# Kernel tuning notes

Hardware: AMD Instinct MI355X
Metric: run time of the kernel (lower is better)

## Reference

```python
import jax, jax.numpy as jnp
import numpy as np

N = 20000        # total atoms (atomic environments)
NFEAT = 2784     # power-spectrum feature size: sum_l n_max[l]^2 * n_pseudo^2
P = 4            # n_pseudo (alchemical pseudo-species)
H = 256          # MLP hidden width
S = 500          # number of structures
NSPEC = 8        # number of chemical species (len(all_species))
AVG_ATOMS = N / S  # average_number_of_atoms used for energy normalization


def setup_inputs() -> dict:
    key = jax.random.key(0)
    ks = jax.random.split(key, 8)
    features = jax.random.normal(ks[0], (N, NFEAT), dtype=jnp.float32)
    species = jax.random.randint(ks[1], (N,), 0, NSPEC)
    structure_idx = jax.random.randint(ks[2], (N,), 0, S)
    # combination matrix: Linear(n_species -> n_pseudo), no bias
    W_comb = jax.random.normal(ks[3], (NSPEC, P), dtype=jnp.float32) / np.float32(np.sqrt(NSPEC))
    # per-pseudo-species MLP weights (bias=False throughout)
    W1 = jax.random.normal(ks[4], (P, NFEAT, H), dtype=jnp.float32) / np.float32(np.sqrt(NFEAT))
    W2 = jax.random.normal(ks[5], (P, H, H), dtype=jnp.float32) / np.float32(np.sqrt(H))
    W3 = jax.random.normal(ks[6], (P, H, H), dtype=jnp.float32) / np.float32(np.sqrt(H))
    W4 = jax.random.normal(ks[7], (P, H, 1), dtype=jnp.float32) / np.float32(np.sqrt(H))
    return {"features": features, "W_comb": W_comb, "W1": W1, "W2": W2,
            "W3": W3, "W4": W4, "species": species, "structure_idx": structure_idx}


def reference(features, W_comb, W1, W2, W3, W4, species, structure_idx):
    # one-hot species encoding followed by combination_matrix linear map.
    # one_hot(species) @ W_comb  ==  W_comb[species]  (gather form, no [N, NSPEC] matmul)
    pseudo_w = W_comb[species]                                   # [N, P]
    # outer-product feature embedding: features[:, :, None] * pseudo_w[:, None, :]
    emb = features[:, :, None] * pseudo_w[:, None, :]            # [N, NFEAT, P]
    # per-pseudo-species MLP (Linear no-bias -> SiLU) x3 -> Linear to scalar,
    # vectorized over the pseudo dimension instead of a Python loop.
    h = jax.nn.silu(jnp.einsum('nfp,pfh->nph', emb, W1))         # [N, P, H]
    h = jax.nn.silu(jnp.einsum('nph,phk->npk', h, W2))           # [N, P, H]
    h = jax.nn.silu(jnp.einsum('nph,phk->npk', h, W3))           # [N, P, H]
    per_pseudo_e = jnp.einsum('nph,pho->npo', h, W4)[..., 0]     # [N, P]
    atomic_energies = per_pseudo_e.sum(axis=1) / np.float32(np.sqrt(P))  # [N]
    # scatter-add atomic energies into per-structure energies (index_add_)
    energies = jax.ops.segment_sum(atomic_energies, structure_idx, num_segments=S)
    return energies / np.float32(AVG_ATOMS)                     # [S]
```

## Files before the change

### kernel.cpp

```cpp
#include <hip/hip_runtime.h>
#include <hip/hip_bf16.h>
#include <stdint.h>

#define N_ATOMS 20000
#define NFEAT   2784
#define KP1     2880
#define KT1     45
#define SS      500
#define NPAD    20224
#define MCOLS   1024

typedef __attribute__((ext_vector_type(8))) short s16x8;
typedef __attribute__((ext_vector_type(4))) float f32x4;

static __device__ __forceinline__ unsigned short f2b(float f) {
    __hip_bfloat16 h = __float2bfloat16(f);
    return __builtin_bit_cast(unsigned short, h);
}
static __device__ __forceinline__ float b2f(unsigned short u) {
    unsigned int x = ((unsigned int)u) << 16;
    return __builtin_bit_cast(float, x);
}

#define GLOAD16(g, l) __builtin_amdgcn_global_load_lds( \
    (const __attribute__((address_space(1))) void*)(g), \
    (__attribute__((address_space(3))) void*)(l), 16, 0, 0)

__global__ void conv_feat(const float* __restrict__ F, unsigned short* __restrict__ out) {
    int row = blockIdx.x;
    int t = threadIdx.x;
    const float4* src = (const float4*)(F + (size_t)row * NFEAT);
    unsigned short* dst = out + (size_t)row * KP1;
    for (int g = t; g < KP1 / 4; g += 256) {
        float4 v;
        if (g < NFEAT / 4) v = src[g];
        else { v.x = 0.f; v.y = 0.f; v.z = 0.f; v.w = 0.f; }
        ushort4 o;
        o.x = f2b(v.x); o.y = f2b(v.y); o.z = f2b(v.z); o.w = f2b(v.w);
        *(ushort4*)(dst + g * 4) = o;
    }
}

__global__ void pack_w(const float* __restrict__ W, unsigned short* __restrict__ Bt,
                       int KD, int KP) {
    __shared__ unsigned short tile[32][256];
    int p = blockIdx.y;
    int f0 = blockIdx.x * 32;
    int t = threadIdx.x;
    #pragma unroll 4
    for (int i = 0; i < 32; ++i) {
        int f = f0 + i;
        float v = (f < KD) ? W[((size_t)p * KD + f) * 256 + t] : 0.f;
        tile[i][t] = f2b(v);
    }
    __syncthreads();
    unsigned short* drow = Bt + (size_t)(p * 256 + t) * KP + f0;
    #pragma unroll
    for (int i = 0; i < 32; i += 4) {
        ushort4 o;
        o.x = tile[i][t]; o.y = tile[i + 1][t]; o.z = tile[i + 2][t]; o.w = tile[i + 3][t];
        *(ushort4*)(drow + i) = o;
    }
}

__global__ void make_pw(const float* __restrict__ Wc, const int* __restrict__ spec,
                        float* __restrict__ pw) {
    int n = blockIdx.x * 256 + threadIdx.x;
    if (n < N_ATOMS) {
        int s = spec[n];
        float4 v = *(const float4*)(Wc + s * 4);
        *(float4*)(pw + n * 4) = v;
    }
}

__global__ void zero_f(float* o, int n) {
    int i = blockIdx.x * 256 + threadIdx.x;
    if (i < n) o[i] = 0.f;
}

__global__ __launch_bounds__(512, 4) void gemm1_pipe(
    const unsigned short* __restrict__ A,
    const unsigned short* __restrict__ Bt,
    const float* __restrict__ pw,
    unsigned short* __restrict__ C)
{
    __shared__ __align__(16) unsigned short lds_a[2 * 8192];
    __shared__ __align__(16) unsigned short lds_b[2 * 8192];

    int bid = blockIdx.x;
    int swz = (bid & 7) * 158 + (bid >> 3);
    int rowTile = swz >> 3;
    int colTile = swz & 7;
    int rowBase = rowTile * 128;
    int colBase = colTile * 128;
    int p = colTile >> 1;

    int t0 = threadIdx.x;
    int wave = t0 >> 6;
    int lane = t0 & 63;
    int wm = wave >> 1;
    int wn = wave & 1;

    int rA = t0 >> 3;
    int ckl = ((t0 & 7) ^ (rA & 7)) << 3;
    const unsigned short* sa = A + (size_t)(rowBase + rA) * KP1 + ckl;
    const unsigned short* sb = Bt + (size_t)(colBase + rA) * KP1 + ckl;

    int ra0 = wm * 32 + (lane & 15);
    int rb0 = wn * 64 + (lane & 15);
    int xr = lane & 7;
    int c0 = lane >> 4;

    f32x4 acc[2][4];
    f32x4 z4 = {0.f, 0.f, 0.f, 0.f};
    #pragma unroll
    for (int i = 0; i < 2; ++i)
        #pragma unroll
        for (int j = 0; j < 4; ++j) acc[i][j] = z4;

#define STAGE1(SB) do { \
    GLOAD16(sa,                     lds_a + (SB) * 8192 + t0 * 8); \
    GLOAD16(sa + (size_t)64 * KP1,  lds_a + (SB) * 8192 + 4096 + t0 * 8); \
    GLOAD16(sb,                     lds_b + (SB) * 8192 + t0 * 8); \
    GLOAD16(sb + (size_t)64 * KP1,  lds_b + (SB) * 8192 + 4096 + t0 * 8); \
    sa += 64; sb += 64; \
} while (0)

    STAGE1(0);
    STAGE1(1);
    asm volatile("s_waitcnt vmcnt(4)" ::: "memory");
    __builtin_amdgcn_s_barrier();
    __builtin_amdgcn_sched_barrier(0);

#define FSTEP(CB) do { \
    s16x8 af[2][2], bv[2][4]; \
    _Pragma("unroll") \
    for (int kk = 0; kk < 2; ++kk) { \
        int ch = ((((kk << 2) | c0) ^ xr) << 3); \
        _Pragma("unroll") \
        for (int fm = 0; fm < 2; ++fm) \
            af[kk][fm] = *(const s16x8*)&lds_a[(CB) * 8192 + (ra0 + fm * 16) * 64 + ch]; \
        _Pragma("unroll") \
        for (int fn = 0; fn < 4; ++fn) \
            bv[kk][fn] = *(const s16x8*)&lds_b[(CB) * 8192 + (rb0 + fn * 16) * 64 + ch]; \
    } \
    asm volatile("s_waitcnt lgkmcnt(0)" ::: "memory"); \
    __builtin_amdgcn_sched_barrier(0); \
    __builtin_amdgcn_s_barrier();             \
    __builtin_amdgcn_sched_barrier(0); \
    STAGE1(CB);                               \
    __builtin_amdgcn_s_setprio(1); \
    _Pragma("unroll") \
    for (int kk = 0; kk < 2; ++kk) \
        _Pragma("unroll") \
        for (int fm = 0; fm < 2; ++fm) \
            _Pragma("unroll") \
            for (int fn = 0; fn < 4; ++fn) \
                acc[fm][fn] = __builtin_amdgcn_mfma_f32_16x16x32_bf16( \
                    af[kk][fm], bv[kk][fn], acc[fm][fn], 0, 0, 0); \
    __builtin_amdgcn_s_setprio(0); \
    asm volatile("s_waitcnt vmcnt(4)" ::: "memory");    \
    __builtin_amdgcn_s_barrier(); \
    __builtin_amdgcn_sched_barrier(0); \
} while (0)

#define TSTEP(CB, DRAIN) do { \
    s16x8 af[2][2], bv[2][4]; \
    _Pragma("unroll") \
    for (int kk = 0; kk < 2; ++kk) { \
        int ch = ((((kk << 2) | c0) ^ xr) << 3); \
        _Pragma("unroll") \
        for (int fm = 0; fm < 2; ++fm) \
            af[kk][fm] = *(const s16x8*)&lds_a[(CB) * 8192 + (ra0 + fm * 16) * 64 + ch]; \
        _Pragma("unroll") \
        for (int fn = 0; fn < 4; ++fn) \
            bv[kk][fn] = *(const s16x8*)&lds_b[(CB) * 8192 + (rb0 + fn * 16) * 64 + ch]; \
    } \
    _Pragma("unroll") \
    for (int kk = 0; kk < 2; ++kk) \
        _Pragma("unroll") \
        for (int fm = 0; fm < 2; ++fm) \
            _Pragma("unroll") \
            for (int fn = 0; fn < 4; ++fn) \
                acc[fm][fn] = __builtin_amdgcn_mfma_f32_16x16x32_bf16( \
                    af[kk][fm], bv[kk][fn], acc[fm][fn], 0, 0, 0); \
    if (DRAIN) { \
        asm volatile("s_waitcnt vmcnt(0)" ::: "memory"); \
        __builtin_amdgcn_s_barrier(); \
        __builtin_amdgcn_sched_barrier(0); \
    } \
} while (0)

    for (int it = 0; it < 21; ++it) {
        FSTEP(0);
        FSTEP(1);
    }
    FSTEP(0);
    TSTEP(1, 1);
    TSTEP(0, 0);
#undef FSTEP
#undef TSTEP
#undef STAGE1

    int rGrp = (lane >> 4) << 2;
    int cLane = lane & 15;
    #pragma unroll
    for (int fm = 0; fm < 2; ++fm) {
        int r0 = rowBase + wm * 32 + fm * 16 + rGrp;
        float pwv[4];
        #pragma unroll
        for (int j = 0; j < 4; ++j) pwv[j] = pw[(size_t)(r0 + j) * 4 + p];
        #pragma unroll
        for (int fn = 0; fn < 4; ++fn) {
            int c = colBase + wn * 64 + fn * 16 + cLane;
            f32x4 a = acc[fm][fn];
            #pragma unroll
            for (int j = 0; j < 4; ++j) {
                float x = a[j] * pwv[j];
                float s = x / (1.f + __expf(-x));
                C[(size_t)(r0 + j) * MCOLS + c] = f2b(s);
            }
        }
    }
}

__global__ __launch_bounds__(256, 2) void mlp_tail(
    const unsigned short* __restrict__ h1,
    const unsigned short* __restrict__ B2t,
    const unsigned short* __restrict__ B3t,
    const float* __restrict__ W4,
    const int* __restrict__ sidx,
    float* __restrict__ out)
{
    __shared__ __align__(16) unsigned short bufA[64 * 256];
    __shared__ __align__(16) unsigned short bufH[64 * 256];

    int bid = blockIdx.x;
    int p  = bid & 3;
    int rg = bid >> 2;
    int r0 = rg * 64;

    int t = threadIdx.x;
    int wave = t >> 6;
    int lane = t & 63;
    int rl = lane & 15;
    int hi = lane >> 4;
    int rGrp = hi << 2;

    {
        int pcs = t & 31;
        #pragma unroll
        for (int i = 0; i < 8; ++i) {
            int row_s = i * 8 + (t >> 5);
            int lcs = (pcs & 24) | ((pcs & 7) ^ (row_s & 7));
            const unsigned short* g =
                h1 + ((size_t)(r0 + row_s) * MCOLS + p * 256 + lcs * 8);
            GLOAD16(g, bufA + i * 2048 + t * 8);
        }
    }
    __syncthreads();

    f32x4 acc[4][4];
    f32x4 z4 = {0.f, 0.f, 0.f, 0.f};

#define LAYER(SRC, BT, DST) do { \
    _Pragma("unroll") \
    for (int i = 0; i < 4; ++i) \
        _Pragma("unroll") \
        for (int j = 0; j < 4; ++j) acc[i][j] = z4; \
    const unsigned short* bp = (BT) + ((size_t)(p * 256 + wave * 64 + rl) * 256); \
    _Pragma("unroll") \
    for (int ks = 0; ks < 8; ++ks) { \
        s16x8 af[4], bv[4]; \
        _Pragma("unroll") \
        for (int fn = 0; fn < 4; ++fn) \
            bv[fn] = *(const s16x8*)(bp + (size_t)fn * 16 * 256 + ks * 32 + hi * 8); \
        _Pragma("unroll") \
        for (int fm = 0; fm < 4; ++fm) { \
            int row = fm * 16 + rl; \
            int lc = ks * 4 + hi; \
            int pc = (lc & 24) | ((lc & 7) ^ (row & 7)); \
            af[fm] = *(const s16x8*)&(SRC)[row * 256 + pc * 8]; \
        } \
        _Pragma("unroll") \
        for (int fm = 0; fm < 4; ++fm) \
            _Pragma("unroll") \
            for (int fn = 0; fn < 4; ++fn) \
                acc[fm][fn] = __builtin_amdgcn_mfma_f32_16x16x32_bf16( \
                    af[fm], bv[fn], acc[fm][fn], 0, 0, 0); \
    } \
     \
     \
     \
    _Pragma("unroll") \
    for (int fm = 0; fm < 4; ++fm) \
        _Pragma("unroll") \
        for (int fn = 0; fn < 4; ++fn) { \
            _Pragma("unroll") \
            for (int j = 0; j < 4; ++j) { \
                int row = fm * 16 + rGrp + j; \
                int col = wave * 64 + fn * 16 + rl; \
                float x = acc[fm][fn][j]; \
                float s = x / (1.f + __expf(-x)); \
                int lc = col >> 3; \
                int pc = (lc & 24) | ((lc & 7) ^ (row & 7)); \
                (DST)[row * 256 + pc * 8 + (col & 7)] = f2b(s); \
            } \
        } \
    __syncthreads(); \
} while (0)

    LAYER(bufA, B2t, bufH);
    LAYER(bufH, B3t, bufA);
#undef LAYER

    {
        int row = t >> 2;
        int q = t & 3;
        const float* w4 = W4 + p * 256;
        float sum = 0.f;
        #pragma unroll
        for (int c = 0; c < 8; ++c) {
            int lc = q * 8 + c;
            int pc = (lc & 24) | ((lc & 7) ^ (row & 7));
            s16x8 v = *(const s16x8*)&bufA[row * 256 + pc * 8];
            #pragma unroll
            for (int e = 0; e < 8; ++e)
                sum += b2f((unsigned short)v[e]) * w4[lc * 8 + e];
        }
        sum += __shfl_down(sum, 2);
        sum += __shfl_down(sum, 1);
        int atom = r0 + row;
        if (q == 0 && atom < N_ATOMS)
            atomicAdd(out + sidx[atom], sum * 0.0125f);
    }
}

extern "C" void kernel_launch(void* const* d_in, const int* in_sizes, int n_in,
                              void* d_out, int out_size, void* d_ws, size_t ws_size,
                              hipStream_t stream) {
    const float* features = (const float*)d_in[0];
    const float* W_comb   = (const float*)d_in[1];
    const float* W1       = (const float*)d_in[2];
    const float* W2       = (const float*)d_in[3];
    const float* W3       = (const float*)d_in[4];
    const float* W4       = (const float*)d_in[5];
    const int*   species  = (const int*)d_in[6];
    const int*   sidx     = (const int*)d_in[7];
    float* out = (float*)d_out;

    char* ws = (char*)d_ws;
    size_t off = 0;
    auto carve = [&](size_t bytes) {
        char* r = ws + off;
        off += (bytes + 255) & ~(size_t)255;
        return r;
    };
    unsigned short* feat = (unsigned short*)carve((size_t)NPAD * KP1 * 2);
    unsigned short* B1t  = (unsigned short*)carve((size_t)1024 * KP1 * 2 + 4096);
    unsigned short* B2t  = (unsigned short*)carve((size_t)1024 * 256 * 2);
    unsigned short* B3t  = (unsigned short*)carve((size_t)1024 * 256 * 2);
    float*          pw   = (float*)carve((size_t)NPAD * 4 * 4);
    unsigned short* h1   = (unsigned short*)carve((size_t)NPAD * 1024 * 2);
    carve(4096);

    conv_feat<<<N_ATOMS, 256, 0, stream>>>(features, feat);
    pack_w<<<dim3(KP1 / 32, 4), 256, 0, stream>>>(W1, B1t, NFEAT, KP1);
    pack_w<<<dim3(8, 4), 256, 0, stream>>>(W2, B2t, 256, 256);
    pack_w<<<dim3(8, 4), 256, 0, stream>>>(W3, B3t, 256, 256);
    make_pw<<<(N_ATOMS + 255) / 256, 256, 0, stream>>>(W_comb, species, pw);
    zero_f<<<2, 256, 0, stream>>>(out, SS);

    gemm1_pipe<<<158 * 8, 512, 0, stream>>>(feat, B1t, pw, h1);
    mlp_tail<<<316 * 4, 256, 0, stream>>>(h1, B2t, B3t, W4, sidx, out);
}
```

Baseline: 328.2 us.

## Halve gemm1 K-step to raise occupancy and merge small prep kernels

The gemm1 pipeline now stages K=32 slices instead of K=64, which halves LDS usage per block and raises the launch-bounds occupancy hint from 4 to 8 blocks. The LDS swizzle and the MFMA inner loop are reworked for the narrower tile, and the loop count doubles to 90 steps. Separately, the W2/W3 packing, pseudo-weight gather and output zeroing are merged into one prep kernel to cut launch overhead. The trade-off is twice as many barriers and load waits per K for the main GEMM, plus shorter global loads per stage.

Result: slower. 833.3 us (+153.9%).

```diff
diff --git a/kernel.cpp b/kernel.cpp
--- a/kernel.cpp
+++ b/kernel.cpp
@@ -5,7 +5,6 @@
 #define N_ATOMS 20000
 #define NFEAT   2784
 #define KP1     2880
-#define KT1     45
 #define SS      500
 #define NPAD    20224
 #define MCOLS   1024
@@ -63,29 +62,52 @@
     }
 }
 
-__global__ void make_pw(const float* __restrict__ Wc, const int* __restrict__ spec,
-                        float* __restrict__ pw) {
-    int n = blockIdx.x * 256 + threadIdx.x;
-    if (n < N_ATOMS) {
-        int s = spec[n];
-        float4 v = *(const float4*)(Wc + s * 4);
-        *(float4*)(pw + n * 4) = v;
-    }
-}
-
-__global__ void zero_f(float* o, int n) {
-    int i = blockIdx.x * 256 + threadIdx.x;
-    if (i < n) o[i] = 0.f;
-}
-
-__global__ __launch_bounds__(512, 4) void gemm1_pipe(
+__global__ void prep_small(const float* __restrict__ W2, const float* __restrict__ W3,
+                           unsigned short* __restrict__ B2t, unsigned short* __restrict__ B3t,
+                           const float* __restrict__ Wc, const int* __restrict__ spec,
+                           float* __restrict__ pw, float* __restrict__ out) {
+    __shared__ unsigned short tile[32][256];
+    int b = blockIdx.x;
+    int t = threadIdx.x;
+    if (b < 64) {
+        const float* W = (b < 32) ? W2 : W3;
+        unsigned short* Bt = (b < 32) ? B2t : B3t;
+        int bb = b & 31;
+        int p = bb >> 3;
+        int f0 = (bb & 7) * 32;
+        #pragma unroll 4
+        for (int i = 0; i < 32; ++i) {
+            int f = f0 + i;
+            tile[i][t] = f2b(W[((size_t)p * 256 + f) * 256 + t]);
+        }
+        __syncthreads();
+        unsigned short* drow = Bt + (size_t)(p * 256 + t) * 256 + f0;
+        #pragma unroll
+        for (int i = 0; i < 32; i += 4) {
+            ushort4 o;
+            o.x = tile[i][t]; o.y = tile[i + 1][t]; o.z = tile[i + 2][t]; o.w = tile[i + 3][t];
+            *(ushort4*)(drow + i) = o;
+        }
+    } else if (b < 143) {
+        int n = (b - 64) * 256 + t;
+        if (n < N_ATOMS) {
+            int s = spec[n];
+            float4 v = *(const float4*)(Wc + s * 4);
+            *(float4*)(pw + n * 4) = v;
+        }
+    } else {
+        for (int i = t; i < SS; i += 256) out[i] = 0.f;
+    }
+}
+
+__global__ __launch_bounds__(512, 8) void gemm1_pipe(
     const unsigned short* __restrict__ A,
     const unsigned short* __restrict__ Bt,
     const float* __restrict__ pw,
     unsigned short* __restrict__ C)
 {
-    __shared__ __align__(16) unsigned short lds_a[2 * 8192];
-    __shared__ __align__(16) unsigned short lds_b[2 * 8192];
+    __shared__ __align__(16) unsigned short lds_a[2 * 4096];
+    __shared__ __align__(16) unsigned short lds_b[2 * 4096];
 
     int bid = blockIdx.x;
     int swz = (bid & 7) * 158 + (bid >> 3);
@@ -101,15 +123,14 @@
     int wm = wave >> 1;
     int wn = wave & 1;
 
-    int rA = t0 >> 3;
-    int ckl = ((t0 & 7) ^ (rA & 7)) << 3;
+    int rA = t0 >> 2;
+    int ckl = ((t0 & 3) ^ (rA & 3)) << 3;
     const unsigned short* sa = A + (size_t)(rowBase + rA) * KP1 + ckl;
     const unsigned short* sb = Bt + (size_t)(colBase + rA) * KP1 + ckl;
 
     int ra0 = wm * 32 + (lane & 15);
     int rb0 = wn * 64 + (lane & 15);
-    int xr = lane & 7;
-    int c0 = lane >> 4;
+    int ch = (((lane >> 4) ^ (lane & 3)) << 3);
 
     f32x4 acc[2][4];
     f32x4 z4 = {0.f, 0.f, 0.f, 0.f};
@@ -119,31 +140,25 @@
         for (int j = 0; j < 4; ++j) acc[i][j] = z4;
 
 #define STAGE1(SB) do { \
-    GLOAD16(sa,                     lds_a + (SB) * 8192 + t0 * 8); \
-    GLOAD16(sa + (size_t)64 * KP1,  lds_a + (SB) * 8192 + 4096 + t0 * 8); \
-    GLOAD16(sb,                     lds_b + (SB) * 8192 + t0 * 8); \
-    GLOAD16(sb + (size_t)64 * KP1,  lds_b + (SB) * 8192 + 4096 + t0 * 8); \
-    sa += 64; sb += 64; \
+    GLOAD16(sa, lds_a + (SB) * 4096 + t0 * 8); \
+    GLOAD16(sb, lds_b + (SB) * 4096 + t0 * 8); \
+    sa += 32; sb += 32; \
 } while (0)
 
     STAGE1(0);
     STAGE1(1);
-    asm volatile("s_waitcnt vmcnt(4)" ::: "memory");
+    asm volatile("s_waitcnt vmcnt(2)" ::: "memory");
     __builtin_amdgcn_s_barrier();
     __builtin_amdgcn_sched_barrier(0);
 
 #define FSTEP(CB) do { \
-    s16x8 af[2][2], bv[2][4]; \
-    _Pragma("unroll") \
-    for (int kk = 0; kk < 2; ++kk) { \
-        int ch = ((((kk << 2) | c0) ^ xr) << 3); \
-        _Pragma("unroll") \
-        for (int fm = 0; fm < 2; ++fm) \
-            af[kk][fm] = *(const s16x8*)&lds_a[(CB) * 8192 + (ra0 + fm * 16) * 64 + ch]; \
-        _Pragma("unroll") \
-        for (int fn = 0; fn < 4; ++fn) \
-            bv[kk][fn] = *(const s16x8*)&lds_b[(CB) * 8192 + (rb0 + fn * 16) * 64 + ch]; \
-    } \
+    s16x8 af[2], bv[4]; \
+    _Pragma("unroll") \
+    for (int fm = 0; fm < 2; ++fm) \
+        af[fm] = *(const s16x8*)&lds_a[(CB) * 4096 + (ra0 + fm * 16) * 32 + ch]; \
+    _Pragma("unroll") \
+    for (int fn = 0; fn < 4; ++fn) \
+        bv[fn] = *(const s16x8*)&lds_b[(CB) * 4096 + (rb0 + fn * 16) * 32 + ch]; \
     asm volatile("s_waitcnt lgkmcnt(0)" ::: "memory"); \
     __builtin_amdgcn_sched_barrier(0); \
     __builtin_amdgcn_s_barrier();             \
@@ -151,39 +166,33 @@
     STAGE1(CB);                               \
     __builtin_amdgcn_s_setprio(1); \
     _Pragma("unroll") \
-    for (int kk = 0; kk < 2; ++kk) \
-        _Pragma("unroll") \
-        for (int fm = 0; fm < 2; ++fm) \
-            _Pragma("unroll") \
-            for (int fn = 0; fn < 4; ++fn) \
-                acc[fm][fn] = __builtin_amdgcn_mfma_f32_16x16x32_bf16( \
-                    af[kk][fm], bv[kk][fn], acc[fm][fn], 0, 0, 0); \
+    for (int fm = 0; fm < 2; ++fm) \
+        _Pragma("unroll") \
+        for (int fn = 0; fn < 4; ++fn) \
+            acc[fm][fn] = __builtin_amdgcn_mfma_f32_16x16x32_bf16( \
+                af[fm], bv[fn], acc[fm][fn], 0, 0, 0); \
     __builtin_amdgcn_s_setprio(0); \
-    asm volatile("s_waitcnt vmcnt(4)" ::: "memory");    \
+    asm volatile("s_waitcnt vmcnt(2)" ::: "memory");    \
     __builtin_amdgcn_s_barrier(); \
     __builtin_amdgcn_sched_barrier(0); \
 } while (0)
 
 #define TSTEP(CB, DRAIN) do { \
-    s16x8 af[2][2], bv[2][4]; \
-    _Pragma("unroll") \
-    for (int kk = 0; kk < 2; ++kk) { \
-        int ch = ((((kk << 2) | c0) ^ xr) << 3); \
-        _Pragma("unroll") \
-        for (int fm = 0; fm < 2; ++fm) \
-            af[kk][fm] = *(const s16x8*)&lds_a[(CB) * 8192 + (ra0 + fm * 16) * 64 + ch]; \
+    s16x8 af[2], bv[4]; \
+    _Pragma("unroll") \
+    for (int fm = 0; fm < 2; ++fm) \
+        af[fm] = *(const s16x8*)&lds_a[(CB) * 4096 + (ra0 + fm * 16) * 32 + ch]; \
+    _Pragma("unroll") \
+    for (int fn = 0; fn < 4; ++fn) \
+        bv[fn] = *(const s16x8*)&lds_b[(CB) * 4096 + (rb0 + fn * 16) * 32 + ch]; \
+    asm volatile("s_waitcnt lgkmcnt(0)" ::: "memory"); \
+    __builtin_amdgcn_sched_barrier(0); \
+    _Pragma("unroll") \
+    for (int fm = 0; fm < 2; ++fm) \
         _Pragma("unroll") \
         for (int fn = 0; fn < 4; ++fn) \
-            bv[kk][fn] = *(const s16x8*)&lds_b[(CB) * 8192 + (rb0 + fn * 16) * 64 + ch]; \
-    } \
-    _Pragma("unroll") \
-    for (int kk = 0; kk < 2; ++kk) \
-        _Pragma("unroll") \
-        for (int fm = 0; fm < 2; ++fm) \
-            _Pragma("unroll") \
-            for (int fn = 0; fn < 4; ++fn) \
-                acc[fm][fn] = __builtin_amdgcn_mfma_f32_16x16x32_bf16( \
-                    af[kk][fm], bv[kk][fn], acc[fm][fn], 0, 0, 0); \
+            acc[fm][fn] = __builtin_amdgcn_mfma_f32_16x16x32_bf16( \
+                af[fm], bv[fn], acc[fm][fn], 0, 0, 0); \
     if (DRAIN) { \
         asm volatile("s_waitcnt vmcnt(0)" ::: "memory"); \
         __builtin_amdgcn_s_barrier(); \
@@ -191,13 +200,12 @@
     } \
 } while (0)
 
-    for (int it = 0; it < 21; ++it) {
+    for (int it = 0; it < 44; ++it) {
         FSTEP(0);
         FSTEP(1);
     }
-    FSTEP(0);
-    TSTEP(1, 1);
-    TSTEP(0, 0);
+    TSTEP(0, 1);
+    TSTEP(1, 0);
 #undef FSTEP
 #undef TSTEP
 #undef STAGE1
@@ -289,9 +297,6 @@
                 acc[fm][fn] = __builtin_amdgcn_mfma_f32_16x16x32_bf16( \
                     af[fm], bv[fn], acc[fm][fn], 0, 0, 0); \
     } \
-     \
-     \
-     \
     _Pragma("unroll") \
     for (int fm = 0; fm < 4; ++fm) \
         _Pragma("unroll") \
@@ -366,10 +371,7 @@
 
     conv_feat<<<N_ATOMS, 256, 0, stream>>>(features, feat);
     pack_w<<<dim3(KP1 / 32, 4), 256, 0, stream>>>(W1, B1t, NFEAT, KP1);
-    pack_w<<<dim3(8, 4), 256, 0, stream>>>(W2, B2t, 256, 256);
-    pack_w<<<dim3(8, 4), 256, 0, stream>>>(W3, B3t, 256, 256);
-    make_pw<<<(N_ATOMS + 255) / 256, 256, 0, stream>>>(W_comb, species, pw);
-    zero_f<<<2, 256, 0, stream>>>(out, SS);
+    prep_small<<<144, 256, 0, stream>>>(W2, W3, B2t, B3t, W_comb, species, pw, out);
 
     gemm1_pipe<<<158 * 8, 512, 0, stream>>>(feat, B1t, pw, h1);
     mlp_tail<<<316 * 4, 256, 0, stream>>>(h1, B2t, B3t, W4, sidx, out);
```
